# Kernel optimization log

Hardware: AMD Instinct MI355X
Metric: run time of the kernel (lower is better)

Reference implementation:

```python
import jax, jax.numpy as jnp
import numpy as np

SEQ_LEN = 2048
N_FFT = 4096  # nearest power of two >= 2*SEQ_LEN - 1
K = 24
D_IN = 512
D_OUT = 512
K_U = 3


def setup_inputs() -> dict:
    key = jax.random.key(0)
    k1, k2, k3, k4, k5 = jax.random.split(key, 5)
    x = jax.random.normal(k1, (1, SEQ_LEN, D_IN), dtype=jnp.float32)
    phi = jax.random.normal(k2, (SEQ_LEN, K), dtype=jnp.float32)
    M = jax.random.normal(k3, (D_OUT, D_IN, K_U), dtype=jnp.float32) / D_IN
    M_phi_plus = jax.random.normal(k4, (K, D_IN, D_OUT), dtype=jnp.float32) / 10.0
    M_phi_minus = jax.random.normal(k5, (K, D_IN, D_OUT), dtype=jnp.float32) / 10.0
    return {"x": x, "phi": phi, "M": M, "M_phi_plus": M_phi_plus, "M_phi_minus": M_phi_minus}


def _convolve(u, v, n):
    # u: (bsz, seq, d_in); v: (seq, K) spectral filters
    bsz, seq_len, d_in = u.shape
    Kf = v.shape[1]
    # alternating sign (+1, -1, +1, ...) along time, shape (1, seq, 1, 1)
    sgn = jnp.where(jnp.arange(seq_len) % 2 == 1, -1.0, 1.0).reshape(1, seq_len, 1, 1)
    v_f = jnp.fft.rfft(v.astype(jnp.float32).reshape(1, seq_len, Kf, 1, 1), n=n, axis=1)
    u_exp = jnp.broadcast_to(u[:, :, None, :], (bsz, seq_len, Kf, d_in))
    # stack [u, u*sgn] -> (bsz, seq, K, d_in, 2)
    U = jnp.stack([u_exp, u_exp * sgn], axis=-1).astype(jnp.float32)
    U_f = jnp.fft.rfft(U, n=n, axis=1)
    U_conv = jnp.fft.irfft(v_f * U_f, n=n, axis=1)[:, :seq_len]
    U_plus = U_conv[..., 0]
    U_minus = U_conv[..., 1] * sgn  # (b, seq, K, d_in) * (1, seq, 1, 1)
    return U_plus, U_minus


def _ar_preds(M, x):
    # M: (d_out, d_in, k_u); x: (b, l, d_in)
    # ar[t] = sum_{i=0}^{k_u-1} M[:,:,i] @ x[t-i]  (zero before start)
    b, l, _ = x.shape
    out = jnp.zeros((b, l, M.shape[0]), dtype=x.dtype)
    for i in range(M.shape[-1]):
        x_shift = jnp.pad(x, ((0, 0), (i, 0), (0, 0)))[:, :l]
        out = out + jnp.einsum("bli,oi->blo", x_shift, M[:, :, i])
    return out


def reference(x, phi, M, M_phi_plus, M_phi_minus):
    U_plus, U_minus = _convolve(x, phi, N_FFT)
    spectral_plus = jnp.einsum("blkd,kdo->blo", U_plus, M_phi_plus)
    spectral_minus = jnp.einsum("blkd,kdo->blo", U_minus, M_phi_minus)
    output = spectral_plus + spectral_minus  # use_hankel_L=False
    ar = _ar_preds(M, x)
    return output + ar
```

## Files before the change

### kernel.cpp

```cpp
#include <hip/hip_runtime.h>

typedef __bf16 bf16;
typedef bf16 bf16x8 __attribute__((ext_vector_type(8)));
typedef float floatx16 __attribute__((ext_vector_type(16)));

#define AS1 __attribute__((address_space(1)))
#define AS3 __attribute__((address_space(3)))

#define KTOT 26112

__device__ __forceinline__ void stage_tile(const bf16* g, int ld, bf16* lds, int tid) {
#pragma unroll
    for (int it = 0; it < 4; ++it) {
        int q    = it * 256 + tid;
        int row  = q >> 3;
        int col8 = (q & 7) ^ (row & 7);
        __builtin_amdgcn_global_load_lds(
            (const AS1 void*)(g + (size_t)row * ld + col8 * 8),
            (AS3 void*)(lds + q * 8), 16, 0, 0);
    }
}

__device__ __forceinline__ void mfma_block(const bf16* lA, const bf16* lB,
                                           floatx16 acc[2][2], int lane, int wm, int wn) {
    const int lrow = lane & 31;
    const int lk   = lane >> 5;
#pragma unroll
    for (int s = 0; s < 4; ++s) {
        bf16x8 af[2], bfr[2];
        const int c8 = s * 2 + lk;
#pragma unroll
        for (int mi = 0; mi < 2; ++mi) {
            int r = wm * 64 + mi * 32 + lrow;
            af[mi] = *(const bf16x8*)(lA + r * 64 + ((c8 ^ (r & 7)) << 3));
        }
#pragma unroll
        for (int ni = 0; ni < 2; ++ni) {
            int r = wn * 64 + ni * 32 + lrow;
            bfr[ni] = *(const bf16x8*)(lB + r * 64 + ((c8 ^ (r & 7)) << 3));
        }
#pragma unroll
        for (int mi = 0; mi < 2; ++mi)
#pragma unroll
            for (int ni = 0; ni < 2; ++ni)
                acc[mi][ni] = __builtin_amdgcn_mfma_f32_32x32x16_bf16(
                    af[mi], bfr[ni], acc[mi][ni], 0, 0, 0);
    }
}

#define CD_ROW(r, lane) (((r) & 3) + 8 * ((r) >> 2) + 4 * ((lane) >> 5))

__global__ __launch_bounds__(256) void conv_gemm(const bf16* __restrict__ Tb,
                                                 const bf16* __restrict__ xT,
                                                 bf16* __restrict__ A2) {
    __shared__ bf16 lA[128 * 64], lB[128 * 64];
    const int tid = threadIdx.x;
    const int lane = tid & 63, wave = tid >> 6, wm = wave & 1, wn = wave >> 1;
    const int bid = blockIdx.x;
    const int a    = 15 - (bid / 192);
    const int rem  = bid % 192;
    const int kf   = rem >> 2;
    const int dblk = rem & 3;

    floatx16 acc[2][2];
#pragma unroll
    for (int mi = 0; mi < 2; ++mi)
#pragma unroll
        for (int ni = 0; ni < 2; ++ni)
#pragma unroll
            for (int e = 0; e < 16; ++e) acc[mi][ni][e] = 0.f;

    for (int c = 0; c <= a; ++c) {
        const bf16* Ab = Tb + ((size_t)kf * 16 + (a - c)) * 16384;
        const bf16* Bb = xT + (size_t)(dblk * 128) * 2048 + c * 128;
#pragma unroll
        for (int kk = 0; kk < 128; kk += 64) {
            stage_tile(Ab + kk, 128, lA, tid);
            stage_tile(Bb + kk, 2048, lB, tid);
            __syncthreads();
            mfma_block(lA, lB, acc, lane, wm, wn);
            __syncthreads();
        }
    }
    bf16* Ob = A2 + (size_t)(a * 128) * KTOT + kf * 512 + dblk * 128;
#pragma unroll
    for (int mi = 0; mi < 2; ++mi)
#pragma unroll
        for (int ni = 0; ni < 2; ++ni)
#pragma unroll
            for (int r = 0; r < 16; ++r) {
                int row = wm * 64 + mi * 32 + CD_ROW(r, lane);
                int col = wn * 64 + ni * 32 + (lane & 31);
                Ob[(size_t)row * KTOT + col] = (bf16)acc[mi][ni][r];
            }
}

__global__ __launch_bounds__(256) void proj_gemm(const bf16* __restrict__ A2,
                                                 const bf16* __restrict__ B2,
                                                 float* __restrict__ P2) {
    __shared__ bf16 lA[128 * 64], lB[128 * 64];
    const int tid = threadIdx.x;
    const int lane = tid & 63, wave = tid >> 6, wm = wave & 1, wn = wave >> 1;
    const int bm = blockIdx.x, sp = blockIdx.y, bn = blockIdx.z;
    const bf16* Ab = A2 + (size_t)bm * 128 * KTOT + sp * 2176;
    const bf16* Bb = B2 + (size_t)bn * 128 * KTOT + sp * 2176;

    floatx16 acc[2][2];
#pragma unroll
    for (int mi = 0; mi < 2; ++mi)
#pragma unroll
        for (int ni = 0; ni < 2; ++ni)
#pragma unroll
            for (int e = 0; e < 16; ++e) acc[mi][ni][e] = 0.f;

    for (int kk = 0; kk < 2176; kk += 64) {
        stage_tile(Ab + kk, KTOT, lA, tid);
        stage_tile(Bb + kk, KTOT, lB, tid);
        __syncthreads();
        mfma_block(lA, lB, acc, lane, wm, wn);
        __syncthreads();
    }
    float* Pt = P2 + (size_t)sp * 1048576;
#pragma unroll
    for (int mi = 0; mi < 2; ++mi)
#pragma unroll
        for (int ni = 0; ni < 2; ++ni)
#pragma unroll
            for (int r = 0; r < 16; ++r) {
                int t = bm * 128 + wm * 64 + mi * 32 + CD_ROW(r, lane);
                int o = bn * 128 + wn * 64 + ni * 32 + (lane & 31);
                Pt[(size_t)t * 512 + o] = acc[mi][ni][r];
            }
}

__global__ void prep_all(const float* __restrict__ x, const float* __restrict__ phi,
                         const float* __restrict__ M, const float* __restrict__ Mp,
                         const float* __restrict__ Mm, bf16* __restrict__ xT,
                         bf16* __restrict__ A2, bf16* __restrict__ B2,
                         bf16* __restrict__ Tb) {
    __shared__ float smem[64 * 65];
    const int b = blockIdx.x, tid = threadIdx.x;
    if (b < 256) {
        int tt = (b >> 3) * 64, dd = (b & 7) * 64;
#pragma unroll
        for (int it = 0; it < 16; ++it) {
            int q = it * 256 + tid;
            int r = q >> 6, cc = q & 63;
            smem[r * 65 + cc] = x[(size_t)(tt + r) * 512 + dd + cc];
        }
        __syncthreads();
#pragma unroll
        for (int it = 0; it < 16; ++it) {
            int q = it * 256 + tid;
            int r = q >> 6, cc = q & 63;
            xT[(size_t)(dd + r) * 2048 + tt + cc] = (bf16)smem[cc * 65 + r];
        }
    } else if (b < 1792) {
        int idx8 = (b - 256) * 256 + tid;
        int t = idx8 / 192, q = idx8 % 192;
        int i = q >> 6, d8 = (q & 63) * 8;
        bf16x8 v;
        if (t - i >= 0) {
            const float* xp = x + (size_t)(t - i) * 512 + d8;
#pragma unroll
            for (int jj = 0; jj < 8; ++jj) v[jj] = (bf16)xp[jj];
        } else {
#pragma unroll
            for (int jj = 0; jj < 8; ++jj) v[jj] = (bf16)0.f;
        }
        *(bf16x8*)(A2 + (size_t)t * KTOT + 24576 + i * 512 + d8) = v;
    } else if (b < 4864) {
        int b2 = b - 1792;
        int kv = b2 >> 6, rem = b2 & 63;
        int dt = (rem >> 3) * 64, ot = (rem & 7) * 64;
        const float* src = (kv < 24) ? (Mp + (size_t)kv * 262144)
                                     : (Mm + (size_t)(kv - 24) * 262144);
#pragma unroll
        for (int it = 0; it < 16; ++it) {
            int q = it * 256 + tid;
            int r = q >> 6, cc = q & 63;
            smem[r * 65 + cc] = src[(size_t)(dt + r) * 512 + ot + cc];
        }
        __syncthreads();
#pragma unroll
        for (int it = 0; it < 16; ++it) {
            int q = it * 256 + tid;
            int r = q >> 6, cc = q & 63;
            B2[(size_t)(ot + r) * KTOT + kv * 512 + dt + cc] = (bf16)smem[cc * 65 + r];
        }
    } else if (b < 5376) {
        int o = b - 4864;
        for (int q = tid; q < 1536; q += 256) smem[q] = M[(size_t)o * 1536 + q];
        __syncthreads();
        for (int q = tid; q < 1536; q += 256) {
            int i = q >> 9, d = q & 511;
            B2[(size_t)o * KTOT + 24576 + q] = (bf16)smem[d * 3 + i];
        }
    } else {
        int b3 = b - 5376;
        int kv = b3 >> 4, m = b3 & 15;
        int k  = (kv >= 24) ? kv - 24 : kv;
        if (tid < 255) {
            int sh = m * 128 - 127 + tid;
            float f = 0.f;
            if (sh >= 0) {
                f = phi[sh * 24 + k];
                if (kv >= 24 && (sh & 1)) f = -f;
            }
            smem[tid] = f;
        }
        __syncthreads();
        bf16* Tp = Tb + (size_t)b3 * 16384;
#pragma unroll
        for (int it = 0; it < 8; ++it) {
            int q = it * 256 + tid;
            int i = q >> 4, j8 = (q & 15) * 8;
            bf16x8 v;
#pragma unroll
            for (int jj = 0; jj < 8; ++jj)
                v[jj] = (bf16)smem[127 + i - (j8 + jj)];
            *(bf16x8*)(Tp + i * 128 + j8) = v;
        }
    }
}

__global__ void reduce12(const float* __restrict__ P2, float* __restrict__ out) {
    int idx = blockIdx.x * 256 + threadIdx.x;
    if (idx >= 2048 * 512) return;
    float s = 0.f;
#pragma unroll
    for (int sp = 0; sp < 12; ++sp)
        s += P2[(size_t)sp * 1048576 + idx];
    out[idx] = s;
}

extern "C" void kernel_launch(void* const* d_in, const int* in_sizes, int n_in,
                              void* d_out, int out_size, void* d_ws, size_t ws_size,
                              hipStream_t stream) {
    const float* x   = (const float*)d_in[0];
    const float* phi = (const float*)d_in[1];
    const float* M   = (const float*)d_in[2];
    const float* Mp  = (const float*)d_in[3];
    const float* Mm  = (const float*)d_in[4];
    float* out = (float*)d_out;
    char* ws = (char*)d_ws;

    bf16*  Tb = (bf16*)(ws + 0);
    bf16*  xT = (bf16*)(ws + 25165824);
    bf16*  A2 = (bf16*)(ws + 27262976);
    bf16*  B2 = (bf16*)(ws + 134217728);
    float* P2 = (float*)(ws + 160956416);

    prep_all<<<6144, 256, 0, stream>>>(x, phi, M, Mp, Mm, xT, A2, B2, Tb);
    conv_gemm<<<3072, 256, 0, stream>>>(Tb, xT, A2);
    proj_gemm<<<dim3(16, 12, 4), 256, 0, stream>>>(A2, B2, P2);
    reduce12<<<4096, 256, 0, stream>>>(P2, out);
}
```

Before: 299.5 us.

## Split Toeplitz conv by parity and fold sign-flipped filters into combined weights

The causal convolution is split into even and odd time polyphase components, so each block-Toeplitz GEMM runs over 1024-length sequences with half the triangular block count per filter. The U_minus branch (sign alternation) is rewritten as a parity selection: conv outputs for each parity are written to the t=2τ+p+w rows and the projection weights become Mp±Mm combinations. This cuts the conv_gemm FLOPs and the Toeplitz tile storage, at the cost of more complex index mapping, boundary masking and an extra zero-fill for the first row region.

```diff
diff --git a/kernel.cpp b/kernel.cpp
--- a/kernel.cpp
+++ b/kernel.cpp
@@ -51,16 +51,16 @@
 #define CD_ROW(r, lane) (((r) & 3) + 8 * ((r) >> 2) + 4 * ((lane) >> 5))
 
 __global__ __launch_bounds__(256) void conv_gemm(const bf16* __restrict__ Tb,
-                                                 const bf16* __restrict__ xT,
+                                                 const bf16* __restrict__ xT2,
                                                  bf16* __restrict__ A2) {
     __shared__ bf16 lA[128 * 64], lB[128 * 64];
     const int tid = threadIdx.x;
     const int lane = tid & 63, wave = tid >> 6, wm = wave & 1, wn = wave >> 1;
     const int bid = blockIdx.x;
-    const int a    = 15 - (bid / 192);
-    const int rem  = bid % 192;
-    const int kf   = rem >> 2;
-    const int dblk = rem & 3;
+    const int a    = 7 - (bid / 384);
+    const int rem  = bid % 384;
+    const int dblk = rem / 48;
+    const int kw   = rem % 48;
 
     floatx16 acc[2][2];
 #pragma unroll
@@ -71,27 +71,33 @@
             for (int e = 0; e < 16; ++e) acc[mi][ni][e] = 0.f;
 
     for (int c = 0; c <= a; ++c) {
-        const bf16* Ab = Tb + ((size_t)kf * 16 + (a - c)) * 16384;
-        const bf16* Bb = xT + (size_t)(dblk * 128) * 2048 + c * 128;
+        const bf16* Ab = Tb + ((size_t)kw * 8 + (a - c)) * 16384;
+        const bf16* Bb = xT2 + (size_t)(dblk * 128) * 1024 + c * 128;
 #pragma unroll
         for (int kk = 0; kk < 128; kk += 64) {
             stage_tile(Ab + kk, 128, lA, tid);
-            stage_tile(Bb + kk, 2048, lB, tid);
+            stage_tile(Bb + kk, 1024, lB, tid);
             __syncthreads();
             mfma_block(lA, lB, acc, lane, wm, wn);
             __syncthreads();
         }
     }
-    bf16* Ob = A2 + (size_t)(a * 128) * KTOT + kf * 512 + dblk * 128;
+    const int w = kw & 1, k = kw >> 1;
+    const int kv = w ? (24 + k) : k;
+    const int p = dblk >> 2, dbase = (dblk & 3) * 128;
+    bf16* Ocol = A2 + (size_t)kv * 512 + dbase;
 #pragma unroll
     for (int mi = 0; mi < 2; ++mi)
 #pragma unroll
         for (int ni = 0; ni < 2; ++ni)
 #pragma unroll
             for (int r = 0; r < 16; ++r) {
-                int row = wm * 64 + mi * 32 + CD_ROW(r, lane);
-                int col = wn * 64 + ni * 32 + (lane & 31);
-                Ob[(size_t)row * KTOT + col] = (bf16)acc[mi][ni][r];
+                int tau = a * 128 + wm * 64 + mi * 32 + CD_ROW(r, lane);
+                int t = 2 * tau + p + w;
+                if (t < 2048) {
+                    int col = wn * 64 + ni * 32 + (lane & 31);
+                    Ocol[(size_t)t * KTOT + col] = (bf16)acc[mi][ni][r];
+                }
             }
 }
 
@@ -135,25 +141,26 @@
 
 __global__ void prep_all(const float* __restrict__ x, const float* __restrict__ phi,
                          const float* __restrict__ M, const float* __restrict__ Mp,
-                         const float* __restrict__ Mm, bf16* __restrict__ xT,
+                         const float* __restrict__ Mm, bf16* __restrict__ xT2,
                          bf16* __restrict__ A2, bf16* __restrict__ B2,
                          bf16* __restrict__ Tb) {
     __shared__ float smem[64 * 65];
     const int b = blockIdx.x, tid = threadIdx.x;
     if (b < 256) {
-        int tt = (b >> 3) * 64, dd = (b & 7) * 64;
-#pragma unroll
-        for (int it = 0; it < 16; ++it) {
-            int q = it * 256 + tid;
-            int r = q >> 6, cc = q & 63;
-            smem[r * 65 + cc] = x[(size_t)(tt + r) * 512 + dd + cc];
-        }
-        __syncthreads();
-#pragma unroll
-        for (int it = 0; it < 16; ++it) {
-            int q = it * 256 + tid;
-            int r = q >> 6, cc = q & 63;
-            xT[(size_t)(dd + r) * 2048 + tt + cc] = (bf16)smem[cc * 65 + r];
+        int dpt = (b >> 4) * 64, st = (b & 15) * 64;
+        int p = dpt >> 9, dbase = dpt & 511;
+#pragma unroll
+        for (int it = 0; it < 16; ++it) {
+            int q = it * 256 + tid;
+            int r = q >> 6, cc = q & 63;
+            smem[r * 65 + cc] = x[(size_t)(2 * (st + r) + p) * 512 + dbase + cc];
+        }
+        __syncthreads();
+#pragma unroll
+        for (int it = 0; it < 16; ++it) {
+            int q = it * 256 + tid;
+            int r = q >> 6, cc = q & 63;
+            xT2[(size_t)(dpt + r) * 1024 + st + cc] = (bf16)smem[cc * 65 + r];
         }
     } else if (b < 1792) {
         int idx8 = (b - 256) * 256 + tid;
@@ -169,45 +176,57 @@
             for (int jj = 0; jj < 8; ++jj) v[jj] = (bf16)0.f;
         }
         *(bf16x8*)(A2 + (size_t)t * KTOT + 24576 + i * 512 + d8) = v;
-    } else if (b < 4864) {
+    } else if (b < 3328) {
         int b2 = b - 1792;
-        int kv = b2 >> 6, rem = b2 & 63;
-        int dt = (rem >> 3) * 64, ot = (rem & 7) * 64;
-        const float* src = (kv < 24) ? (Mp + (size_t)kv * 262144)
-                                     : (Mm + (size_t)(kv - 24) * 262144);
-#pragma unroll
-        for (int it = 0; it < 16; ++it) {
-            int q = it * 256 + tid;
-            int r = q >> 6, cc = q & 63;
-            smem[r * 65 + cc] = src[(size_t)(dt + r) * 512 + ot + cc];
-        }
-        __syncthreads();
-#pragma unroll
-        for (int it = 0; it < 16; ++it) {
-            int q = it * 256 + tid;
-            int r = q >> 6, cc = q & 63;
-            B2[(size_t)(ot + r) * KTOT + kv * 512 + dt + cc] = (bf16)smem[cc * 65 + r];
-        }
-    } else if (b < 5376) {
-        int o = b - 4864;
+        int k = b2 >> 6, rem2 = b2 & 63;
+        int dt = (rem2 >> 3) * 64, ot = (rem2 & 7) * 64;
+        const float* Sp = Mp + (size_t)k * 262144;
+        const float* Sm = Mm + (size_t)k * 262144;
+#pragma unroll
+        for (int it = 0; it < 16; ++it) {
+            int q = it * 256 + tid;
+            int r = q >> 6, cc = q & 63;
+            smem[r * 65 + cc] = Sp[(size_t)(dt + r) * 512 + ot + cc];
+        }
+        __syncthreads();
+        float m1[16];
+#pragma unroll
+        for (int it = 0; it < 16; ++it) {
+            int q = it * 256 + tid;
+            int r = q >> 6, cc = q & 63;
+            m1[it] = smem[cc * 65 + r];
+        }
+        __syncthreads();
+#pragma unroll
+        for (int it = 0; it < 16; ++it) {
+            int q = it * 256 + tid;
+            int r = q >> 6, cc = q & 63;
+            smem[r * 65 + cc] = Sm[(size_t)(dt + r) * 512 + ot + cc];
+        }
+        __syncthreads();
+#pragma unroll
+        for (int it = 0; it < 16; ++it) {
+            int q = it * 256 + tid;
+            int r = q >> 6, cc = q & 63;
+            float m2 = smem[cc * 65 + r];
+            B2[(size_t)(ot + r) * KTOT + k * 512 + dt + cc]        = (bf16)(m1[it] + m2);
+            B2[(size_t)(ot + r) * KTOT + (24 + k) * 512 + dt + cc] = (bf16)(m1[it] - m2);
+        }
+    } else if (b < 3840) {
+        int o = b - 3328;
         for (int q = tid; q < 1536; q += 256) smem[q] = M[(size_t)o * 1536 + q];
         __syncthreads();
         for (int q = tid; q < 1536; q += 256) {
             int i = q >> 9, d = q & 511;
             B2[(size_t)o * KTOT + 24576 + q] = (bf16)smem[d * 3 + i];
         }
-    } else {
-        int b3 = b - 5376;
-        int kv = b3 >> 4, m = b3 & 15;
-        int k  = (kv >= 24) ? kv - 24 : kv;
+    } else if (b < 4224) {
+        int b3 = b - 3840;
+        int kw = b3 >> 3, m = b3 & 7;
+        int k = kw >> 1, w = kw & 1;
         if (tid < 255) {
             int sh = m * 128 - 127 + tid;
-            float f = 0.f;
-            if (sh >= 0) {
-                f = phi[sh * 24 + k];
-                if (kv >= 24 && (sh & 1)) f = -f;
-            }
-            smem[tid] = f;
+            smem[tid] = (sh >= 0) ? phi[(size_t)(2 * sh + w) * 24 + k] : 0.f;
         }
         __syncthreads();
         bf16* Tp = Tb + (size_t)b3 * 16384;
@@ -221,6 +240,12 @@
                 v[jj] = (bf16)smem[127 + i - (j8 + jj)];
             *(bf16x8*)(Tp + i * 128 + j8) = v;
         }
+    } else {
+        int off = 12288 + (b - 4224) * 2048 + tid * 8;
+        bf16x8 z;
+#pragma unroll
+        for (int jj = 0; jj < 8; ++jj) z[jj] = (bf16)0.f;
+        *(bf16x8*)(A2 + off) = z;
     }
 }
 
@@ -245,14 +270,14 @@
     float* out = (float*)d_out;
     char* ws = (char*)d_ws;
 
-    bf16*  Tb = (bf16*)(ws + 0);
-    bf16*  xT = (bf16*)(ws + 25165824);
-    bf16*  A2 = (bf16*)(ws + 27262976);
-    bf16*  B2 = (bf16*)(ws + 134217728);
-    float* P2 = (float*)(ws + 160956416);
-
-    prep_all<<<6144, 256, 0, stream>>>(x, phi, M, Mp, Mm, xT, A2, B2, Tb);
-    conv_gemm<<<3072, 256, 0, stream>>>(Tb, xT, A2);
+    bf16*  Tb  = (bf16*)(ws + 0);
+    bf16*  xT2 = (bf16*)(ws + 12582912);
+    bf16*  A2  = (bf16*)(ws + 14680064);
+    bf16*  B2  = (bf16*)(ws + 121634816);
+    float* P2  = (float*)(ws + 148373504);
+
+    prep_all<<<4230, 256, 0, stream>>>(x, phi, M, Mp, Mm, xT2, A2, B2, Tb);
+    conv_gemm<<<3072, 256, 0, stream>>>(Tb, xT2, A2);
     proj_gemm<<<dim3(16, 12, 4), 256, 0, stream>>>(A2, B2, P2);
     reduce12<<<4096, 256, 0, stream>>>(P2, out);
 }
```

Measured after the change: 269.1 us. 1.11x faster.
